# Optimization experiments

Hardware: AMD Instinct MI355X
Metric: run time of the kernel (lower is better)

Reference implementation:

```python
import jax, jax.numpy as jnp
import numpy as np

ANNEALING_SCALE = 0.1
BS, NV, S, D, V = 2, 16, 1024, 768, 50257

def setup_inputs() -> dict:
    key = jax.random.key(0)
    k1, k2, k3, k4, k5 = jax.random.split(key, 5)
    return {
        "input_ids": jax.random.randint(k1, (BS, S), 0, V),
        "content": jax.random.normal(k2, (BS, NV, S, D), dtype=jnp.float32),
        "contextualization": jax.random.normal(k3, (BS, NV, S, S), dtype=jnp.float32) * 0.05,
        "lm_head_weight": jax.random.normal(k4, (V, D), dtype=jnp.float32) * 0.02,
        "content_weights": jax.random.uniform(k5, (V, NV), dtype=jnp.float32),
    }

def reference(input_ids, content, contextualization, lm_head_weight, content_weights):
    bs, nv, s, d = content.shape
    # --- mask_annealing ---
    # Original computes relu(content @ W.T) over full vocab then gathers at input_ids.
    # Equivalent: gather rows of W first, then contract (same math since relu is
    # elementwise and only gathered columns are summed).
    Wg = lm_head_weight[input_ids]                              # (bs, s, d)
    sims = jnp.einsum('bkid,bjd->bkij', content, Wg)            # (bs, 16, s, s)
    sims = jnp.sum(jax.nn.relu(sims), axis=3)                   # (bs, 16, s)
    scores = jax.nn.sigmoid(-ANNEALING_SCALE * sims + 6.0)
    # upweight_nearby modifier
    scores = scores * (1.0 + jnp.arange(s, dtype=content.dtype) / 100.0)[None, None, :]
    scores = jnp.transpose(scores, (0, 2, 1))                   # (bs, s, 16)
    # --- create_content_soft_mask ---
    cw = content_weights[input_ids]                             # (bs, s, 16)
    weights = cw * scores + (1.0 - scores)                      # (bs, s, 16)
    # --- weighted sense combination ---
    content_m = content * jnp.transpose(weights, (0, 2, 1))[..., None]  # (bs,16,s,d)
    hidden = jnp.einsum('bkij,bkjd->bid', contextualization, content_m) # (bs, s, d)
    logits = hidden @ lm_head_weight.T                          # (bs, s, vocab)
    return logits
```

## Files before the change

### kernel.cpp

```cpp
#include <hip/hip_runtime.h>
#include <cstdint>
#include <cstddef>

#define BSZ 2
#define NV 16
#define SEQ 1024
#define DIM 768
#define VOC 50257
#define VOCP 50304

typedef unsigned int u32;
typedef unsigned short u16;
typedef _Float16 half8 __attribute__((ext_vector_type(8)));
typedef float f32x4 __attribute__((ext_vector_type(4)));

__device__ __forceinline__ u16 f2h(float f) {
  return __builtin_bit_cast(unsigned short, (_Float16)f);
}
__device__ __forceinline__ u32 pk2h(float a, float b) {
  return (u32)f2h(a) | ((u32)f2h(b) << 16);
}

__device__ __forceinline__ void gload16(const u16* g, u16* l) {
  __builtin_amdgcn_global_load_lds(
      (const __attribute__((address_space(1))) void*)g,
      (__attribute__((address_space(3))) void*)l, 16, 0, 0);
}

__global__ void k_prep_content(const float* __restrict__ content,
                               u16* __restrict__ cbf, u16* __restrict__ cT) {
  __shared__ u16 tile[32][33];
  const int bk = blockIdx.z;
  const int d0 = blockIdx.x * 32, j0 = blockIdx.y * 32;
  const float* src = content + (size_t)bk * SEQ * DIM;
  u16* dst = cbf + (size_t)bk * SEQ * DIM;
  u16* dstT = cT + (size_t)bk * DIM * SEQ;
  const int c = threadIdx.x;
#pragma unroll
  for (int rr = 0; rr < 4; ++rr) {
    const int r = threadIdx.y * 4 + rr;
    const float v = src[(size_t)(j0 + r) * DIM + d0 + c];
    const u16 bv = f2h(v);
    dst[(size_t)(j0 + r) * DIM + d0 + c] = bv;
    tile[r][c] = bv;
  }
  __syncthreads();
#pragma unroll
  for (int rr = 0; rr < 4; ++rr) {
    const int r = threadIdx.y * 4 + rr;
    dstT[(size_t)(d0 + r) * SEQ + j0 + c] = tile[c][r];
  }
}

__global__ void k_prep_w(const float* __restrict__ W, u16* __restrict__ Wb) {
  const int v = blockIdx.x;
  const int c = threadIdx.x * 4;
  u32 lo, hi;
  if (v < VOC) {
    const float4 f = *(const float4*)(W + (size_t)v * DIM + c);
    lo = pk2h(f.x, f.y); hi = pk2h(f.z, f.w);
  } else {
    lo = 0u; hi = 0u;
  }
  *(uint2*)(Wb + (size_t)v * DIM + c) = make_uint2(lo, hi);
}

__global__ void k_gather(const int* __restrict__ ids, const u16* __restrict__ Wb,
                         u16* __restrict__ Wg) {
  const int b = blockIdx.y, j = blockIdx.x;
  const int row = ids[b * SEQ + j];
  const int c = threadIdx.x * 4;
  *(uint2*)(Wg + ((size_t)b * SEQ + j) * DIM + c) =
      *(const uint2*)(Wb + (size_t)row * DIM + c);
}

__global__ void k_zero(float* __restrict__ p, int n) {
  const int i = blockIdx.x * 256 + threadIdx.x;
  if (i < n) p[i] = 0.f;
}

template <int LDA, int LDB>
__device__ __forceinline__ void gemm_ktile(const u16* __restrict__ A,
                                           const u16* __restrict__ B, int ksteps,
                                           u16* As, u16* Bs, f32x4 (&acc)[4][4],
                                           int t) {
  const int lane = t & 63, w = t >> 6, wr = w >> 1, wc = w & 1;
  const int kl = (lane >> 4) * 8, rl = lane & 15;
  const int srow = t >> 2;
  const int scol = (t & 3) * 8;
  u16* lA = As + w * 512;
  u16* lB = Bs + w * 512;
  const u16* ga = A + (size_t)srow * LDA + scol;
  const u16* gb = B + (size_t)srow * LDB + scol;
  for (int kt = 0; kt < ksteps; ++kt) {
    __syncthreads();
    gload16(ga, lA);
    gload16(ga + (size_t)64 * LDA, lA + 2048);
    gload16(gb, lB);
    gload16(gb + (size_t)64 * LDB, lB + 2048);
    ga += 32; gb += 32;
    __syncthreads();
    half8 af[4], bf[4];
#pragma unroll
    for (int m = 0; m < 4; ++m)
      af[m] = *(const half8*)(As + (wr * 64 + m * 16 + rl) * 32 + kl);
#pragma unroll
    for (int n = 0; n < 4; ++n)
      bf[n] = *(const half8*)(Bs + (wc * 64 + n * 16 + rl) * 32 + kl);
#pragma unroll
    for (int m = 0; m < 4; ++m)
#pragma unroll
      for (int n = 0; n < 4; ++n)
        acc[m][n] = __builtin_amdgcn_mfma_f32_16x16x32_f16(af[m], bf[n], acc[m][n], 0, 0, 0);
  }
}

__global__ __launch_bounds__(256) void k_sims(const u16* __restrict__ cbf,
                                              const u16* __restrict__ Wg,
                                              float* __restrict__ sims) {
  __shared__ __align__(16) u16 As[128 * 32];
  __shared__ __align__(16) u16 Bs[128 * 32];
  const int bk = blockIdx.z, b = bk >> 4;
  const int t = threadIdx.x;
  const u16* A = cbf + (size_t)bk * SEQ * DIM + (size_t)(blockIdx.y * 128) * DIM;
  const u16* B = Wg + (size_t)b * SEQ * DIM + (size_t)(blockIdx.x * 128) * DIM;
  f32x4 acc[4][4] = {};
  gemm_ktile<DIM, DIM>(A, B, DIM / 32, As, Bs, acc, t);
  const int lane = t & 63, w = t >> 6, wr = w >> 1;
  const int rg = lane >> 4, cl = lane & 15;
#pragma unroll
  for (int m = 0; m < 4; ++m) {
#pragma unroll
    for (int r = 0; r < 4; ++r) {
      float s = 0.f;
#pragma unroll
      for (int n = 0; n < 4; ++n) {
        const float v = acc[m][n][r];
        s += fmaxf(v, 0.f);
      }
      s += __shfl_xor(s, 1);
      s += __shfl_xor(s, 2);
      s += __shfl_xor(s, 4);
      s += __shfl_xor(s, 8);
      if (cl == 0) {
        const int i = blockIdx.y * 128 + wr * 64 + m * 16 + rg * 4 + r;
        atomicAdd(&sims[(size_t)bk * SEQ + i], s);
      }
    }
  }
}

__global__ void k_weights(const float* __restrict__ sims, const int* __restrict__ ids,
                          const float* __restrict__ cw, float* __restrict__ wtsT) {
  const int j = blockIdx.x * 256 + threadIdx.x;
  const int bk = blockIdx.y;
  const int b = bk >> 4, k = bk & 15;
  const float sm = sims[(size_t)bk * SEQ + j];
  float score = 1.f / (1.f + __expf(0.1f * sm - 6.f));
  score *= 1.f + (float)j * 0.01f;
  const int id = ids[b * SEQ + j];
  const float c = cw[(size_t)id * NV + k];
  wtsT[(size_t)bk * SEQ + j] = c * score + (1.f - score);
}

__global__ void k_ctx(const float* __restrict__ ctx, const float* __restrict__ wtsT,
                      u16* __restrict__ ctxw) {
  const size_t i = ((size_t)blockIdx.x * 256 + threadIdx.x) * 4;
  const float4 c = *(const float4*)(ctx + i);
  const size_t bk = i >> 20;
  const int j = (int)(i & (SEQ - 1));
  const float4 wv = *(const float4*)(wtsT + bk * SEQ + j);
  *(uint2*)(ctxw + i) =
      make_uint2(pk2h(c.x * wv.x, c.y * wv.y), pk2h(c.z * wv.z, c.w * wv.w));
}

__global__ __launch_bounds__(256) void k_hidden(const u16* __restrict__ ctxw,
                                                const u16* __restrict__ cT,
                                                float* __restrict__ part) {
  __shared__ __align__(16) u16 As[128 * 32];
  __shared__ __align__(16) u16 Bs[128 * 32];
  const int z = blockIdx.z;
  const int b = z >> 2, g = z & 3;
  const int i0 = blockIdx.y * 128, d0 = blockIdx.x * 128;
  const int t = threadIdx.x;
  f32x4 acc[4][4] = {};
  for (int kk = 0; kk < 4; ++kk) {
    const int sense = g * 4 + kk;
    const u16* A = ctxw + ((size_t)(b * NV + sense) * SEQ + i0) * SEQ;
    const u16* B = cT + ((size_t)(b * NV + sense) * DIM + d0) * SEQ;
    gemm_ktile<SEQ, SEQ>(A, B, SEQ / 32, As, Bs, acc, t);
  }
  const int lane = t & 63, w = t >> 6, wr = w >> 1, wc = w & 1;
  const int rg = lane >> 4, cl = lane & 15;
  float* P = part + ((size_t)(g * BSZ + b) * SEQ + i0) * DIM + d0;
#pragma unroll
  for (int m = 0; m < 4; ++m)
#pragma unroll
    for (int n = 0; n < 4; ++n)
#pragma unroll
      for (int r = 0; r < 4; ++r)
        P[(size_t)(wr * 64 + m * 16 + rg * 4 + r) * DIM + wc * 64 + n * 16 + cl] =
            acc[m][n][r];
}

__global__ void k_reduce(const float* __restrict__ part, u16* __restrict__ hid) {
  const size_t i = ((size_t)blockIdx.x * 256 + threadIdx.x) * 4;
  const size_t NHID = (size_t)BSZ * SEQ * DIM;
  float4 s = {0.f, 0.f, 0.f, 0.f};
#pragma unroll
  for (int g = 0; g < 4; ++g) {
    const float4 p = *(const float4*)(part + (size_t)g * NHID + i);
    s.x += p.x; s.y += p.y; s.z += p.z; s.w += p.w;
  }
  *(uint2*)(hid + i) = make_uint2(pk2h(s.x, s.y), pk2h(s.z, s.w));
}

__global__ __launch_bounds__(256) void k_logits(const u16* __restrict__ hid,
                                                const u16* __restrict__ Wb,
                                                float* __restrict__ out) {
  __shared__ __align__(16) u16 As[128 * 32];
  __shared__ __align__(16) u16 Bs[128 * 32];
  const int i0 = blockIdx.x * 128, v0 = blockIdx.y * 128;
  const int t = threadIdx.x;
  const u16* A = hid + (size_t)i0 * DIM;
  const u16* B = Wb + (size_t)v0 * DIM;
  f32x4 acc[4][4] = {};
  gemm_ktile<DIM, DIM>(A, B, DIM / 32, As, Bs, acc, t);
  const int lane = t & 63, w = t >> 6, wr = w >> 1, wc = w & 1;
  const int rg = lane >> 4, cl = lane & 15;
#pragma unroll
  for (int m = 0; m < 4; ++m)
#pragma unroll
    for (int n = 0; n < 4; ++n) {
      const int vv = v0 + wc * 64 + n * 16 + cl;
      if (vv < VOC) {
#pragma unroll
        for (int r = 0; r < 4; ++r) {
          const int i = i0 + wr * 64 + m * 16 + rg * 4 + r;
          out[(size_t)i * VOC + vv] = acc[m][n][r];
        }
      }
    }
}

extern "C" void kernel_launch(void* const* d_in, const int* in_sizes, int n_in,
                              void* d_out, int out_size, void* d_ws, size_t ws_size,
                              hipStream_t stream) {
  const int* ids = (const int*)d_in[0];
  const float* content = (const float*)d_in[1];
  const float* ctx = (const float*)d_in[2];
  const float* W = (const float*)d_in[3];
  const float* cw = (const float*)d_in[4];
  float* out = (float*)d_out;
  char* ws = (char*)d_ws;

  u16* cbf  = (u16*)(ws);
  u16* cT   = (u16*)(ws + 50331648);
  u16* Wb   = (u16*)(ws + 100663296);
  u16* Wg   = (u16*)(ws + 177930240);
  u16* ctxw = (u16*)(ws + 181075968);
  float* sims = (float*)(ws + 248184832);
  float* wtsT = (float*)(ws + 248315904);
  float* part = (float*)cbf;
  u16* hid = Wg;

  k_prep_content<<<dim3(DIM / 32, SEQ / 32, BSZ * NV), dim3(32, 8), 0, stream>>>(
      content, cbf, cT);
  k_prep_w<<<VOCP, 192, 0, stream>>>(W, Wb);
  k_gather<<<dim3(SEQ, BSZ), 192, 0, stream>>>(ids, Wb, Wg);
  k_zero<<<128, 256, 0, stream>>>(sims, BSZ * NV * SEQ);
  k_sims<<<dim3(8, 8, BSZ * NV), 256, 0, stream>>>(cbf, Wg, sims);
  k_weights<<<dim3(4, BSZ * NV), 256, 0, stream>>>(sims, ids, cw, wtsT);
  k_ctx<<<32768, 256, 0, stream>>>(ctx, wtsT, ctxw);
  k_hidden<<<dim3(6, 8, 8), 256, 0, stream>>>(ctxw, cT, part);
  k_reduce<<<1536, 256, 0, stream>>>(part, hid);
  k_logits<<<dim3(16, 393), 256, 0, stream>>>(hid, Wb, out);
}
```

Measured before the change: 669.1 us.

## Double-buffer GEMM LDS tiles with swizzled layout and XCD-aware block remap

Replaces the single-buffered GEMM k-loop with a double-buffered one: the async global-to-LDS load for the next k-tile is issued before computing the current one, leaving one barrier per step instead of two. The LDS column offsets are XOR-swizzled to cut bank conflicts on fragment reads. The logits kernel switches to a 1-D grid with a remap intended to group tiles sharing weight rows on the same XCD. This doubles LDS use per block, which may lower occupancy.

```diff
diff --git a/kernel.cpp b/kernel.cpp
--- a/kernel.cpp
+++ b/kernel.cpp
@@ -80,52 +80,68 @@
 }
 
 template <int LDA, int LDB>
-__device__ __forceinline__ void gemm_ktile(const u16* __restrict__ A,
-                                           const u16* __restrict__ B, int ksteps,
-                                           u16* As, u16* Bs, f32x4 (&acc)[4][4],
-                                           int t) {
+__device__ __forceinline__ void gemm_core(const u16* __restrict__ A,
+                                          const u16* __restrict__ B, int ksteps,
+                                          u16* As, u16* Bs, f32x4 (&acc)[4][4],
+                                          int t) {
   const int lane = t & 63, w = t >> 6, wr = w >> 1, wc = w & 1;
-  const int kl = (lane >> 4) * 8, rl = lane & 15;
-  const int srow = t >> 2;
-  const int scol = (t & 3) * 8;
+  const int rl = lane & 15;
+  const int gsw = (((lane >> 4) ^ ((rl >> 1) & 3)) * 8);
+  const int srow = 16 * w + (lane >> 2);
+  const int sg = (((lane & 3) ^ ((lane >> 3) & 3)) * 8);
+  const size_t gaBase = (size_t)srow * LDA + sg;
+  const size_t gbBase = (size_t)srow * LDB + sg;
   u16* lA = As + w * 512;
   u16* lB = Bs + w * 512;
-  const u16* ga = A + (size_t)srow * LDA + scol;
-  const u16* gb = B + (size_t)srow * LDB + scol;
-  for (int kt = 0; kt < ksteps; ++kt) {
+
+#define STAGE_(bb, kt)                                                  \
+  {                                                                     \
+    const u16* ga_ = A + gaBase + (size_t)(kt) * 32;                    \
+    const u16* gb_ = B + gbBase + (size_t)(kt) * 32;                    \
+    gload16(ga_, lA + (bb) * 4096);                                     \
+    gload16(ga_ + (size_t)64 * LDA, lA + (bb) * 4096 + 2048);           \
+    gload16(gb_, lB + (bb) * 4096);                                     \
+    gload16(gb_ + (size_t)64 * LDB, lB + (bb) * 4096 + 2048);           \
+  }
+
+#define FRAGS_(bb)                                                      \
+  half8 af[4], bf[4];                                                   \
+  _Pragma("unroll") for (int m = 0; m < 4; ++m)                         \
+      af[m] = *(const half8*)(As + (bb) * 4096 +                        \
+                              (wr * 64 + m * 16 + rl) * 32 + gsw);      \
+  _Pragma("unroll") for (int n = 0; n < 4; ++n)                         \
+      bf[n] = *(const half8*)(Bs + (bb) * 4096 +                        \
+                              (wc * 64 + n * 16 + rl) * 32 + gsw);      \
+  _Pragma("unroll") for (int m = 0; m < 4; ++m)                         \
+      _Pragma("unroll") for (int n = 0; n < 4; ++n)                     \
+          acc[m][n] = __builtin_amdgcn_mfma_f32_16x16x32_f16(           \
+              af[m], bf[n], acc[m][n], 0, 0, 0);
+
+  STAGE_(0, 0);
+  __syncthreads();
+  int cur = 0;
+  for (int kt = 0; kt < ksteps - 1; ++kt) {
+    STAGE_(cur ^ 1, kt + 1);
+    { FRAGS_(cur); }
     __syncthreads();
-    gload16(ga, lA);
-    gload16(ga + (size_t)64 * LDA, lA + 2048);
-    gload16(gb, lB);
-    gload16(gb + (size_t)64 * LDB, lB + 2048);
-    ga += 32; gb += 32;
-    __syncthreads();
-    half8 af[4], bf[4];
-#pragma unroll
-    for (int m = 0; m < 4; ++m)
-      af[m] = *(const half8*)(As + (wr * 64 + m * 16 + rl) * 32 + kl);
-#pragma unroll
-    for (int n = 0; n < 4; ++n)
-      bf[n] = *(const half8*)(Bs + (wc * 64 + n * 16 + rl) * 32 + kl);
-#pragma unroll
-    for (int m = 0; m < 4; ++m)
-#pragma unroll
-      for (int n = 0; n < 4; ++n)
-        acc[m][n] = __builtin_amdgcn_mfma_f32_16x16x32_f16(af[m], bf[n], acc[m][n], 0, 0, 0);
-  }
+    cur ^= 1;
+  }
+  { FRAGS_(cur); }
+#undef STAGE_
+#undef FRAGS_
 }
 
 __global__ __launch_bounds__(256) void k_sims(const u16* __restrict__ cbf,
                                               const u16* __restrict__ Wg,
                                               float* __restrict__ sims) {
-  __shared__ __align__(16) u16 As[128 * 32];
-  __shared__ __align__(16) u16 Bs[128 * 32];
+  __shared__ __align__(16) u16 As[2 * 128 * 32];
+  __shared__ __align__(16) u16 Bs[2 * 128 * 32];
   const int bk = blockIdx.z, b = bk >> 4;
   const int t = threadIdx.x;
   const u16* A = cbf + (size_t)bk * SEQ * DIM + (size_t)(blockIdx.y * 128) * DIM;
   const u16* B = Wg + (size_t)b * SEQ * DIM + (size_t)(blockIdx.x * 128) * DIM;
   f32x4 acc[4][4] = {};
-  gemm_ktile<DIM, DIM>(A, B, DIM / 32, As, Bs, acc, t);
+  gemm_core<DIM, DIM>(A, B, DIM / 32, As, Bs, acc, t);
   const int lane = t & 63, w = t >> 6, wr = w >> 1;
   const int rg = lane >> 4, cl = lane & 15;
 #pragma unroll
@@ -177,8 +193,8 @@
 __global__ __launch_bounds__(256) void k_hidden(const u16* __restrict__ ctxw,
                                                 const u16* __restrict__ cT,
                                                 float* __restrict__ part) {
-  __shared__ __align__(16) u16 As[128 * 32];
-  __shared__ __align__(16) u16 Bs[128 * 32];
+  __shared__ __align__(16) u16 As[2 * 128 * 32];
+  __shared__ __align__(16) u16 Bs[2 * 128 * 32];
   const int z = blockIdx.z;
   const int b = z >> 2, g = z & 3;
   const int i0 = blockIdx.y * 128, d0 = blockIdx.x * 128;
@@ -188,7 +204,8 @@
     const int sense = g * 4 + kk;
     const u16* A = ctxw + ((size_t)(b * NV + sense) * SEQ + i0) * SEQ;
     const u16* B = cT + ((size_t)(b * NV + sense) * DIM + d0) * SEQ;
-    gemm_ktile<SEQ, SEQ>(A, B, SEQ / 32, As, Bs, acc, t);
+    gemm_core<SEQ, SEQ>(A, B, SEQ / 32, As, Bs, acc, t);
+    __syncthreads();
   }
   const int lane = t & 63, w = t >> 6, wr = w >> 1, wc = w & 1;
   const int rg = lane >> 4, cl = lane & 15;
@@ -218,14 +235,17 @@
 __global__ __launch_bounds__(256) void k_logits(const u16* __restrict__ hid,
                                                 const u16* __restrict__ Wb,
                                                 float* __restrict__ out) {
-  __shared__ __align__(16) u16 As[128 * 32];
-  __shared__ __align__(16) u16 Bs[128 * 32];
-  const int i0 = blockIdx.x * 128, v0 = blockIdx.y * 128;
+  __shared__ __align__(16) u16 As[2 * 128 * 32];
+  __shared__ __align__(16) u16 Bs[2 * 128 * 32];
+  const int nwg = 16 * 393;
+  const int bid = blockIdx.x;
+  const int swz = (bid & 7) * (nwg / 8) + (bid >> 3);
+  const int i0 = (swz & 15) * 128, v0 = (swz >> 4) * 128;
   const int t = threadIdx.x;
   const u16* A = hid + (size_t)i0 * DIM;
   const u16* B = Wb + (size_t)v0 * DIM;
   f32x4 acc[4][4] = {};
-  gemm_ktile<DIM, DIM>(A, B, DIM / 32, As, Bs, acc, t);
+  gemm_core<DIM, DIM>(A, B, DIM / 32, As, Bs, acc, t);
   const int lane = t & 63, w = t >> 6, wr = w >> 1, wc = w & 1;
   const int rg = lane >> 4, cl = lane & 15;
 #pragma unroll
@@ -274,5 +294,5 @@
   k_ctx<<<32768, 256, 0, stream>>>(ctx, wtsT, ctxw);
   k_hidden<<<dim3(6, 8, 8), 256, 0, stream>>>(ctxw, cT, part);
   k_reduce<<<1536, 256, 0, stream>>>(part, hid);
-  k_logits<<<dim3(16, 393), 256, 0, stream>>>(hid, Wb, out);
-}
+  k_logits<<<16 * 393, 256, 0, stream>>>(hid, Wb, out);
+}
```

Result: faster. 634.5 us (-5.2%).
